# Kernel optimization log

Measured on AMD Instinct MI355X. Metric: run time of the kernel, lower is better.

Reference implementation:

```python
import jax, jax.numpy as jnp
import numpy as np

N = 65536        # total points across batch
NS = 16          # nsample (kNN neighbors)
D = 64           # d_model
FF = 64          # dim_feedforward width
CIN = 16         # input feature channels
EPS = 1e-5       # BatchNorm eps


def _bn_relu(x, g, b):
    # BatchNorm1d in training mode: per-channel stats over (N, L); x: (N, C, L)
    m = x.mean(axis=(0, 2), keepdims=True)
    v = x.var(axis=(0, 2), keepdims=True)
    return jax.nn.relu((x - m) * jax.lax.rsqrt(v + EPS) * g[None, :, None] + b[None, :, None])


def _dknn_layer(xyz, feats, knn_idx, knn_empty,
                wq, bq, wk, bk, w1, g1, b1, w2, g2, b2, wo, go, bo):
    # nhead = 1 -> single head uses the full d_model split
    Q = feats @ wq + bq                        # (N, D)
    K = feats @ wk + bk                        # (N, D)
    Kx = jnp.concatenate([K, xyz], axis=1)     # use_xyz=True -> (N, D+3)
    Qx = jnp.concatenate([Q, xyz], axis=1)     # (N, D+3)
    Kg = jnp.transpose(Kx[knn_idx], (0, 2, 1))  # irregular gather -> (N, D+3, NS)
    Qe = Qx[:, :, None]                        # (N, D+3, 1)
    x = jnp.concatenate([Kg - Qe, jnp.broadcast_to(Qe, Kg.shape)], axis=1)  # (N, 2*(D+3), NS)
    x = jnp.where(knn_empty[:, None, None], 0.0, x)   # empty-ball masking
    x = _bn_relu(jnp.einsum('ncs,cf->nfs', x, w1), g1, b1)  # Conv1d k=1 == channel matmul
    x = _bn_relu(jnp.einsum('ncs,cf->nfs', x, w2), g2, b2)
    x = jnp.max(x, axis=2, keepdims=True)      # max-pool over neighbors -> (N, FF, 1)
    x = _bn_relu(jnp.einsum('ncs,cf->nfs', x, wo), go, bo)  # out_conv
    return x[:, :, 0]                          # (N, D)


def setup_inputs() -> dict:
    key = jax.random.key(0)
    ks = jax.random.split(key, 16)
    inp = {
        'src_xyz': jax.random.normal(ks[0], (N, 3), jnp.float32) * 20.0,
        'src_feats': jax.random.normal(ks[1], (N, CIN), jnp.float32),
        'knn_idx': jax.random.randint(ks[2], (N, NS), 0, N, jnp.int32),
        'knn_empty': jax.random.randint(ks[3], (N,), 0, 20, jnp.int32) == 0,
    }
    k = 4
    cin = CIN
    for i in range(2):
        s = 1.0 / np.sqrt(cin)
        inp[f'l{i}_wq'] = jax.random.normal(ks[k], (cin, D), jnp.float32) * s; k += 1
        inp[f'l{i}_bq'] = jnp.zeros((D,), jnp.float32)
        inp[f'l{i}_wk'] = jax.random.normal(ks[k], (cin, D), jnp.float32) * s; k += 1
        inp[f'l{i}_bk'] = jnp.zeros((D,), jnp.float32)
        c = 2 * (D + 3)
        inp[f'l{i}_w1'] = jax.random.normal(ks[k], (c, FF), jnp.float32) * np.sqrt(2.0 / c); k += 1
        inp[f'l{i}_g1'] = jnp.ones((FF,), jnp.float32)
        inp[f'l{i}_b1'] = jnp.zeros((FF,), jnp.float32)
        inp[f'l{i}_w2'] = jax.random.normal(ks[k], (FF, FF), jnp.float32) * np.sqrt(2.0 / FF); k += 1
        inp[f'l{i}_g2'] = jnp.ones((FF,), jnp.float32)
        inp[f'l{i}_b2'] = jnp.zeros((FF,), jnp.float32)
        inp[f'l{i}_wo'] = jax.random.normal(ks[k], (FF, D), jnp.float32) * np.sqrt(2.0 / FF); k += 1
        inp[f'l{i}_go'] = jnp.ones((D,), jnp.float32)
        inp[f'l{i}_bo'] = jnp.zeros((D,), jnp.float32)
        cin = D
    return inp


def reference(src_xyz, src_feats, knn_idx, knn_empty,
              l0_wq, l0_bq, l0_wk, l0_bk, l0_w1, l0_g1, l0_b1, l0_w2, l0_g2, l0_b2, l0_wo, l0_go, l0_bo,
              l1_wq, l1_bq, l1_wk, l1_bk, l1_w1, l1_g1, l1_b1, l1_w2, l1_g2, l1_b2, l1_wo, l1_go, l1_bo):
    f = _dknn_layer(src_xyz, src_feats, knn_idx, knn_empty,
                    l0_wq, l0_bq, l0_wk, l0_bk, l0_w1, l0_g1, l0_b1, l0_w2, l0_g2, l0_b2, l0_wo, l0_go, l0_bo)
    f = _dknn_layer(src_xyz, f, knn_idx, knn_empty,
                    l1_wq, l1_bq, l1_wk, l1_bk, l1_w1, l1_g1, l1_b1, l1_w2, l1_g2, l1_b2, l1_wo, l1_go, l1_bo)
    return f
```

## Files before the change

kernel.cpp:

```cpp
#include <hip/hip_runtime.h>
#include <cstdint>

#define NPTS 65536
#define NS 16
#define EPSV 1e-5f

typedef __attribute__((ext_vector_type(8))) short bf16x8;
typedef __attribute__((ext_vector_type(4))) float f32x4;
typedef __attribute__((ext_vector_type(4))) unsigned int u32x4;
union FragU { u32x4 u; bf16x8 h; };

#define SUM1 0
#define SSQ1 64
#define SUM2 128
#define SSQ2 192
#define SUM3 256
#define SSQ3 320
#define WKAOF 0
#define WQBAOF 4096
#define BKAOF 8192
#define BQBAOF 8256
#define WFOLD_FLOATS 8320

__device__ __forceinline__ int permc(int c) {
    int t = c >> 5, g = (c >> 3) & 3, i = c & 7;
    return (t*2 + (i>>2))*16 + g*4 + (i&3);
}

__device__ __forceinline__ void split2(float e0, float e1, unsigned int& hi, unsigned int& lo) {
    unsigned int u0 = __float_as_uint(e0), u1 = __float_as_uint(e1);
    hi = __builtin_amdgcn_perm(u1, u0, 0x07060302u);
    float l0f = e0 - __uint_as_float(u0 & 0xFFFF0000u);
    float l1f = e1 - __uint_as_float(u1 & 0xFFFF0000u);
    lo = __builtin_amdgcn_perm(__float_as_uint(l1f), __float_as_uint(l0f), 0x07060302u);
}

__global__ void k_mask(const uint32_t* emp32, uint8_t* mask) {
    int bad = 0;
    for (int w = threadIdx.x; w < 1024; w += 256) bad |= (emp32[w] > 1u) ? 1 : 0;
    __shared__ int sbad[4];
    unsigned long long b = __ballot(bad != 0);
    if ((threadIdx.x & 63) == 0) sbad[threadIdx.x >> 6] = (b != 0ull) ? 1 : 0;
    __syncthreads();
    int flag = sbad[0] | sbad[1] | sbad[2] | sbad[3];
    int i = blockIdx.x * 256 + threadIdx.x;
    uint8_t mv;
    if (flag) mv = (((const uint8_t*)emp32)[i] != 0);
    else      mv = (emp32[i] != 0u);
    mask[i] = mv;
}

__global__ void k0(const float* wq, const float* bq, const float* wk, const float* bk,
                   const float* w1, float* wfold, int cin) {
    int f = threadIdx.x;
    int c = blockIdx.x;
    float a = 0.f, q = 0.f;
    for (int d = 0; d < 64; d++) {
        float A  = w1[d*64 + f];
        float Bm = w1[(67+d)*64 + f] - A;
        a = fmaf(wk[c*64 + d], A,  a);
        q = fmaf(wq[c*64 + d], Bm, q);
    }
    wfold[WKAOF  + c*64 + f] = a;
    wfold[WQBAOF + c*64 + f] = q;
    if (c == 0) {
        float ba = 0.f, bqv = 0.f;
        for (int d = 0; d < 64; d++) {
            float A  = w1[d*64 + f];
            float Bm = w1[(67+d)*64 + f] - A;
            ba  = fmaf(bk[d], A,  ba);
            bqv = fmaf(bq[d], Bm, bqv);
        }
        wfold[BKAOF  + f] = ba;
        wfold[BQBAOF + f] = bqv;
    }
}

template<int CIN, bool PREBN>
__global__ void __launch_bounds__(256) k1m(const float* __restrict__ feats, const float* __restrict__ xyz,
                    const float* __restrict__ w1, const float* __restrict__ wfold,
                    const float* __restrict__ statsPrev, const float* __restrict__ goP,
                    const float* __restrict__ boP,
                    float* __restrict__ KA, float* __restrict__ QBA) {
    const int l = threadIdx.x & 63;
    const int wv = threadIdx.x >> 6;
    const int sidx = l & 15;
    const int g = l >> 4;
    const int col = sidx;
    constexpr int NT = (CIN == 64) ? 2 : 1;

    unsigned int bh[NT][2][4], bl[NT][2][4];
    #pragma unroll
    for (int t = 0; t < NT; t++)
    #pragma unroll
    for (int fl = 0; fl < 2; fl++) {
        int f128 = (wv*2 + fl)*16 + col;
        const float* W = (f128 < 64) ? (wfold + WKAOF) : (wfold + WQBAOF);
        int f = (f128 < 64) ? f128 : f128 - 64;
        #pragma unroll
        for (int r = 0; r < 4; r++) {
            int c0 = t*32 + g*8 + 2*r;
            float e0 = 0.f, e1 = 0.f;
            if (CIN == 64 || g < 2) {
                e0 = W[c0*64 + f];
                e1 = W[(c0+1)*64 + f];
            }
            split2(e0, e1, bh[t][fl][r], bl[t][fl][r]);
        }
    }
    unsigned int xbh[2][4], xbl[2][4];
    float biasf[2];
    int posO[2];
    #pragma unroll
    for (int fl = 0; fl < 2; fl++) {
        int f128 = (wv*2 + fl)*16 + col;
        float A0, A1, A2;
        if (f128 < 64) {
            A0 = w1[64*64 + f128]; A1 = w1[65*64 + f128]; A2 = w1[66*64 + f128];
            biasf[fl] = wfold[BKAOF + f128];
            posO[fl] = permc(f128);
        } else {
            int f = f128 - 64;
            A0 = w1[131*64 + f] - w1[64*64 + f];
            A1 = w1[132*64 + f] - w1[65*64 + f];
            A2 = w1[133*64 + f] - w1[66*64 + f];
            biasf[fl] = wfold[BQBAOF + f];
            posO[fl] = permc(f);
        }
        split2(A0, A1, xbh[fl][0], xbl[fl][0]);
        split2(A2, 0.f, xbh[fl][1], xbl[fl][1]);
        xbh[fl][2] = 0; xbh[fl][3] = 0; xbl[fl][2] = 0; xbl[fl][3] = 0;
    }
    float scP[NT*8], shP[NT*8];
    if (PREBN) {
        const float invN = 1.0f / (float)NPTS;
        #pragma unroll
        for (int t = 0; t < NT; t++)
        #pragma unroll
        for (int i = 0; i < 8; i++) {
            int c = t*32 + g*8 + i;
            float m = statsPrev[SUM3 + c] * invN;
            float v = fmaxf(statsPrev[SSQ3 + c] * invN - m*m, 0.0f);
            float s = goP[c] * rsqrtf(v + EPSV);
            scP[t*8+i] = s;
            shP[t*8+i] = fmaf(-m, s, boP[c]);
        }
    }

    for (int tile = blockIdx.x; tile < NPTS/16; tile += gridDim.x) {
        int p = tile*16 + sidx;
        unsigned int ahu[NT][4], alu[NT][4];
        #pragma unroll
        for (int t = 0; t < NT; t++) {
            float xv[8];
            if (CIN == 64) {
                f32x4 a0 = *(const f32x4*)(feats + (size_t)p*64 + t*32 + g*8);
                f32x4 a1 = *(const f32x4*)(feats + (size_t)p*64 + t*32 + g*8 + 4);
                #pragma unroll
                for (int i = 0; i < 4; i++) { xv[i] = a0[i]; xv[4+i] = a1[i]; }
                if (PREBN) {
                    #pragma unroll
                    for (int i = 0; i < 8; i++)
                        xv[i] = fmaxf(fmaf(scP[t*8+i], xv[i], shP[t*8+i]), 0.0f);
                }
            } else {
                if (g < 2) {
                    f32x4 a0 = *(const f32x4*)(feats + (size_t)p*16 + g*8);
                    f32x4 a1 = *(const f32x4*)(feats + (size_t)p*16 + g*8 + 4);
                    #pragma unroll
                    for (int i = 0; i < 4; i++) { xv[i] = a0[i]; xv[4+i] = a1[i]; }
                } else {
                    #pragma unroll
                    for (int i = 0; i < 8; i++) xv[i] = 0.f;
                }
            }
            #pragma unroll
            for (int r = 0; r < 4; r++) split2(xv[2*r], xv[2*r+1], ahu[t][r], alu[t][r]);
        }
        unsigned int xah[4] = {0,0,0,0}, xal[4] = {0,0,0,0};
        if (g == 0) {
            float x0 = xyz[p*3], x1 = xyz[p*3+1], x2 = xyz[p*3+2];
            split2(x0, x1, xah[0], xal[0]);
            split2(x2, 0.f, xah[1], xal[1]);
        }
        f32x4 acc[2];
        #pragma unroll
        for (int fl = 0; fl < 2; fl++)
            acc[fl] = (f32x4){biasf[fl], biasf[fl], biasf[fl], biasf[fl]};
        #pragma unroll
        for (int t = 0; t < NT; t++) {
            FragU ah, al;
            ah.u = (u32x4){ahu[t][0], ahu[t][1], ahu[t][2], ahu[t][3]};
            al.u = (u32x4){alu[t][0], alu[t][1], alu[t][2], alu[t][3]};
            #pragma unroll
            for (int fl = 0; fl < 2; fl++) {
                FragU Bh, Bl;
                Bh.u = (u32x4){bh[t][fl][0], bh[t][fl][1], bh[t][fl][2], bh[t][fl][3]};
                Bl.u = (u32x4){bl[t][fl][0], bl[t][fl][1], bl[t][fl][2], bl[t][fl][3]};
                acc[fl] = __builtin_amdgcn_mfma_f32_16x16x32_bf16(ah.h, Bh.h, acc[fl], 0, 0, 0);
                acc[fl] = __builtin_amdgcn_mfma_f32_16x16x32_bf16(ah.h, Bl.h, acc[fl], 0, 0, 0);
                acc[fl] = __builtin_amdgcn_mfma_f32_16x16x32_bf16(al.h, Bh.h, acc[fl], 0, 0, 0);
            }
        }
        {
            FragU ah, al;
            ah.u = (u32x4){xah[0], xah[1], xah[2], xah[3]};
            al.u = (u32x4){xal[0], xal[1], xal[2], xal[3]};
            #pragma unroll
            for (int fl = 0; fl < 2; fl++) {
                FragU Bh, Bl;
                Bh.u = (u32x4){xbh[fl][0], xbh[fl][1], xbh[fl][2], xbh[fl][3]};
                Bl.u = (u32x4){xbl[fl][0], xbl[fl][1], xbl[fl][2], xbl[fl][3]};
                acc[fl] = __builtin_amdgcn_mfma_f32_16x16x32_bf16(ah.h, Bh.h, acc[fl], 0, 0, 0);
                acc[fl] = __builtin_amdgcn_mfma_f32_16x16x32_bf16(ah.h, Bl.h, acc[fl], 0, 0, 0);
                acc[fl] = __builtin_amdgcn_mfma_f32_16x16x32_bf16(al.h, Bh.h, acc[fl], 0, 0, 0);
            }
        }
        #pragma unroll
        for (int fl = 0; fl < 2; fl++) {
            int f128 = (wv*2 + fl)*16 + col;
            #pragma unroll
            for (int r = 0; r < 4; r++) {
                int po = tile*16 + g*4 + r;
                float v = acc[fl][r];
                if (f128 < 64) KA[(size_t)po*64 + posO[fl]] = v;
                else           QBA[(size_t)po*64 + posO[fl]] = v;
            }
        }
    }
}

__global__ void __launch_bounds__(256) k2(const float* __restrict__ KA, const float* __restrict__ QBA,
                   const int* __restrict__ knn, const uint8_t* __restrict__ mask, float* stats) {
    const int l = threadIdx.x & 63;
    const int wv = threadIdx.x >> 6;
    const int s = l & 15;
    const int g = l >> 4;
    float s0[16], s1[16];
    #pragma unroll
    for (int i = 0; i < 16; i++) { s0[i] = 0.f; s1[i] = 0.f; }

    const int STR = gridDim.x * 8;
    for (int n0 = blockIdx.x * 8 + wv*2; n0 < NPTS; n0 += STR) {
        bool msk[2];
        f32x4 ka[2][4];
        #pragma unroll
        for (int u = 0; u < 2; u++) {
            int n = n0 + u;
            msk[u] = (mask[n] != 0);
            if (!msk[u]) {
                int j = knn[n*16 + s];
                const float* kap = KA + (size_t)j*64 + g*4;
                #pragma unroll
                for (int q = 0; q < 4; q++) ka[u][q] = *(const f32x4*)(kap + q*16);
            }
        }
        #pragma unroll
        for (int u = 0; u < 2; u++) {
            if (msk[u]) continue;
            int n = n0 + u;
            const float* qbp = QBA + (size_t)n*64 + g*4;
            #pragma unroll
            for (int q = 0; q < 4; q++) {
                f32x4 qb = *(const f32x4*)(qbp + q*16);
                #pragma unroll
                for (int e = 0; e < 4; e++) {
                    float y = ka[u][q][e] + qb[e];
                    s0[q*4+e] += y;
                    s1[q*4+e] = fmaf(y, y, s1[q*4+e]);
                }
            }
        }
    }
    #pragma unroll
    for (int i = 0; i < 16; i++) {
        #pragma unroll
        for (int d = 1; d < 16; d <<= 1) {
            s0[i] += __shfl_xor(s0[i], d, 64);
            s1[i] += __shfl_xor(s1[i], d, 64);
        }
    }
    __shared__ float r0[4][64], r1[4][64];
    if (s == 0) {
        #pragma unroll
        for (int q = 0; q < 4; q++)
        #pragma unroll
        for (int e = 0; e < 4; e++) {
            int c = (q>>1)*32 + g*8 + (q&1)*4 + e;
            r0[wv][c] = s0[q*4+e];
            r1[wv][c] = s1[q*4+e];
        }
    }
    __syncthreads();
    int tid = threadIdx.x;
    if (tid < 64) {
        atomicAdd(&stats[SUM1 + tid], r0[0][tid]+r0[1][tid]+r0[2][tid]+r0[3][tid]);
        atomicAdd(&stats[SSQ1 + tid], r1[0][tid]+r1[1][tid]+r1[2][tid]+r1[3][tid]);
    }
}

__global__ void __launch_bounds__(256) k4(const float* __restrict__ KA, const float* __restrict__ QBA,
                   const int* __restrict__ knn, const uint8_t* __restrict__ mask,
                   const float* __restrict__ w2, const float* __restrict__ g1, const float* __restrict__ b1,
                   float* stats, float* __restrict__ y2max, float* __restrict__ y2min) {
    const int l    = threadIdx.x & 63;
    const int wv   = threadIdx.x >> 6;
    const int sidx = l & 15;
    const int g    = l >> 4;
    const int col  = sidx;

    float sc1v[16], sh1v[16];
    const float inv = 1.0f / ((float)NPTS * (float)NS);
    #pragma unroll
    for (int t = 0; t < 2; t++)
    #pragma unroll
    for (int i = 0; i < 8; i++) {
        int c = t*32 + g*8 + i;
        float m = stats[SUM1 + c] * inv;
        float v = fmaxf(stats[SSQ1 + c] * inv - m*m, 0.0f);
        float s = g1[c] * rsqrtf(v + EPSV);
        sc1v[t*8+i] = s;
        sh1v[t*8+i] = fmaf(-m, s, b1[c]);
    }

    unsigned int whu[2][4][4], wlu[2][4][4];
    #pragma unroll
    for (int t = 0; t < 2; t++)
    #pragma unroll
    for (int ft = 0; ft < 4; ft++)
    #pragma unroll
    for (int r = 0; r < 4; r++) {
        int k0i = t*32 + g*8 + 2*r;
        float e0 = w2[k0i*64 + ft*16 + col];
        float e1 = w2[(k0i+1)*64 + ft*16 + col];
        split2(e0, e1, whu[t][ft][r], wlu[t][ft][r]);
    }

    float s0t[4] = {0.f,0.f,0.f,0.f};
    float s1t[4] = {0.f,0.f,0.f,0.f};

    const int STR = gridDim.x * 8;
    for (int n0 = blockIdx.x * 8 + wv*2; n0 < NPTS; n0 += STR) {
        bool msk[2];
        f32x4 ka[2][4];
        #pragma unroll
        for (int u = 0; u < 2; u++) {
            int n = n0 + u;
            msk[u] = (mask[n] != 0);
            int j = knn[n*16 + sidx];
            const float* kap = KA + (size_t)j*64 + g*4;
            #pragma unroll
            for (int q = 0; q < 4; q++) ka[u][q] = *(const f32x4*)(kap + q*16);
        }
        #pragma unroll
        for (int u = 0; u < 2; u++) {
            int n = n0 + u;
            bool masked = msk[u];
            const float* qbp = QBA + (size_t)n*64 + g*4;
            f32x4 qq[4];
            #pragma unroll
            for (int q = 0; q < 4; q++) qq[q] = *(const f32x4*)(qbp + q*16);

            float x[16];
            #pragma unroll
            for (int t = 0; t < 2; t++)
            #pragma unroll
            for (int i = 0; i < 8; i++) {
                int q = t*2 + (i>>2), r = i&3;
                float y = masked ? 0.f : (ka[u][q][r] + qq[q][r]);
                x[t*8+i] = fmaxf(fmaf(sc1v[t*8+i], y, sh1v[t*8+i]), 0.0f);
            }

            unsigned int ahu[2][4], alu[2][4];
            #pragma unroll
            for (int t = 0; t < 2; t++)
            #pragma unroll
            for (int r = 0; r < 4; r++)
                split2(x[t*8 + 2*r], x[t*8 + 2*r + 1], ahu[t][r], alu[t][r]);

            f32x4 acc[4];
            #pragma unroll
            for (int ft = 0; ft < 4; ft++) acc[ft] = (f32x4){0.f,0.f,0.f,0.f};

            #pragma unroll
            for (int t = 0; t < 2; t++) {
                FragU ah, al;
                ah.u = (u32x4){ahu[t][0], ahu[t][1], ahu[t][2], ahu[t][3]};
                al.u = (u32x4){alu[t][0], alu[t][1], alu[t][2], alu[t][3]};
                #pragma unroll
                for (int ft = 0; ft < 4; ft++) {
                    FragU bhf, blf;
                    bhf.u = (u32x4){whu[t][ft][0], whu[t][ft][1], whu[t][ft][2], whu[t][ft][3]};
                    blf.u = (u32x4){wlu[t][ft][0], wlu[t][ft][1], wlu[t][ft][2], wlu[t][ft][3]};
                    acc[ft] = __builtin_amdgcn_mfma_f32_16x16x32_bf16(ah.h, bhf.h, acc[ft], 0, 0, 0);
                    acc[ft] = __builtin_amdgcn_mfma_f32_16x16x32_bf16(ah.h, blf.h, acc[ft], 0, 0, 0);
                    acc[ft] = __builtin_amdgcn_mfma_f32_16x16x32_bf16(al.h, bhf.h, acc[ft], 0, 0, 0);
                }
            }

            float tmax[4], tmin[4];
            #pragma unroll
            for (int ft = 0; ft < 4; ft++) {
                f32x4 d = acc[ft];
                float lmax = fmaxf(fmaxf(d[0], d[1]), fmaxf(d[2], d[3]));
                float lmin = fminf(fminf(d[0], d[1]), fminf(d[2], d[3]));
                s0t[ft] += (d[0] + d[1]) + (d[2] + d[3]);
                s1t[ft] += fmaf(d[0],d[0], fmaf(d[1],d[1], fmaf(d[2],d[2], d[3]*d[3])));
                lmax = fmaxf(lmax, __shfl_xor(lmax, 16, 64));
                lmax = fmaxf(lmax, __shfl_xor(lmax, 32, 64));
                lmin = fminf(lmin, __shfl_xor(lmin, 16, 64));
                lmin = fminf(lmin, __shfl_xor(lmin, 32, 64));
                tmax[ft] = lmax; tmin[ft] = lmin;
            }
            float mx = (g==0) ? tmax[0] : (g==1) ? tmax[1] : (g==2) ? tmax[2] : tmax[3];
            float mn = (g==0) ? tmin[0] : (g==1) ? tmin[1] : (g==2) ? tmin[2] : tmin[3];
            y2max[(size_t)n*64 + l] = mx;
            y2min[(size_t)n*64 + l] = mn;
        }
    }

    #pragma unroll
    for (int ft = 0; ft < 4; ft++) {
        s0t[ft] += __shfl_xor(s0t[ft], 16, 64);
        s0t[ft] += __shfl_xor(s0t[ft], 32, 64);
        s1t[ft] += __shfl_xor(s1t[ft], 16, 64);
        s1t[ft] += __shfl_xor(s1t[ft], 32, 64);
    }
    float myS0 = (g==0) ? s0t[0] : (g==1) ? s0t[1] : (g==2) ? s0t[2] : s0t[3];
    float myS1 = (g==0) ? s1t[0] : (g==1) ? s1t[1] : (g==2) ? s1t[2] : s1t[3];
    __shared__ float red[8][64];
    red[wv][l] = myS0;
    red[4+wv][l] = myS1;
    __syncthreads();
    if (wv == 0) {
        atomicAdd(&stats[SUM2 + l], red[0][l]+red[1][l]+red[2][l]+red[3][l]);
        atomicAdd(&stats[SSQ2 + l], red[4][l]+red[5][l]+red[6][l]+red[7][l]);
    }
}

__global__ void __launch_bounds__(256) k5m(const float* __restrict__ y2max, const float* __restrict__ y2min,
                    const float* __restrict__ wo, const float* __restrict__ g2, const float* __restrict__ b2,
                    float* stats, float* __restrict__ y3) {
    const int l = threadIdx.x & 63;
    const int wv = threadIdx.x >> 6;
    const int sidx = l & 15;
    const int g = l >> 4;
    const int ft = wv;

    unsigned int bh[2][4], bl[2][4];
    #pragma unroll
    for (int t = 0; t < 2; t++)
    #pragma unroll
    for (int r = 0; r < 4; r++) {
        int c0 = t*32 + g*8 + 2*r;
        split2(wo[c0*64 + ft*16 + sidx], wo[(c0+1)*64 + ft*16 + sidx], bh[t][r], bl[t][r]);
    }
    float sc2v[16], sh2v[16];
    const float inv = 1.0f / ((float)NPTS * (float)NS);
    #pragma unroll
    for (int t = 0; t < 2; t++)
    #pragma unroll
    for (int i = 0; i < 8; i++) {
        int c = t*32 + g*8 + i;
        float m = stats[SUM2 + c] * inv;
        float v = fmaxf(stats[SSQ2 + c] * inv - m*m, 0.0f);
        float s = g2[c] * rsqrtf(v + EPSV);
        sc2v[t*8+i] = s;
        sh2v[t*8+i] = fmaf(-m, s, b2[c]);
    }
    float s0a = 0.f, s1a = 0.f;
    for (int tile = blockIdx.x; tile < NPTS/16; tile += gridDim.x) {
        int p = tile*16 + sidx;
        unsigned int ahu[2][4], alu[2][4];
        #pragma unroll
        for (int t = 0; t < 2; t++) {
            f32x4 mx0 = *(const f32x4*)(y2max + (size_t)p*64 + t*32 + g*8);
            f32x4 mx1 = *(const f32x4*)(y2max + (size_t)p*64 + t*32 + g*8 + 4);
            f32x4 mn0 = *(const f32x4*)(y2min + (size_t)p*64 + t*32 + g*8);
            f32x4 mn1 = *(const f32x4*)(y2min + (size_t)p*64 + t*32 + g*8 + 4);
            float mval[8];
            #pragma unroll
            for (int i = 0; i < 4; i++) {
                float sc = sc2v[t*8+i];
                float pre = (sc >= 0.f) ? mx0[i] : mn0[i];
                mval[i] = fmaxf(fmaf(sc, pre, sh2v[t*8+i]), 0.0f);
                float sc2 = sc2v[t*8+4+i];
                float pre2 = (sc2 >= 0.f) ? mx1[i] : mn1[i];
                mval[4+i] = fmaxf(fmaf(sc2, pre2, sh2v[t*8+4+i]), 0.0f);
            }
            #pragma unroll
            for (int r = 0; r < 4; r++) split2(mval[2*r], mval[2*r+1], ahu[t][r], alu[t][r]);
        }
        f32x4 acc = (f32x4){0.f,0.f,0.f,0.f};
        #pragma unroll
        for (int t = 0; t < 2; t++) {
            FragU ah, al, Bh, Bl;
            ah.u = (u32x4){ahu[t][0], ahu[t][1], ahu[t][2], ahu[t][3]};
            al.u = (u32x4){alu[t][0], alu[t][1], alu[t][2], alu[t][3]};
            Bh.u = (u32x4){bh[t][0], bh[t][1], bh[t][2], bh[t][3]};
            Bl.u = (u32x4){bl[t][0], bl[t][1], bl[t][2], bl[t][3]};
            acc = __builtin_amdgcn_mfma_f32_16x16x32_bf16(ah.h, Bh.h, acc, 0, 0, 0);
            acc = __builtin_amdgcn_mfma_f32_16x16x32_bf16(ah.h, Bl.h, acc, 0, 0, 0);
            acc = __builtin_amdgcn_mfma_f32_16x16x32_bf16(al.h, Bh.h, acc, 0, 0, 0);
        }
        #pragma unroll
        for (int r = 0; r < 4; r++) {
            int po = tile*16 + g*4 + r;
            float v = acc[r];
            y3[(size_t)po*64 + ft*16 + sidx] = v;
            s0a += v;
            s1a = fmaf(v, v, s1a);
        }
    }
    s0a += __shfl_xor(s0a, 16, 64); s0a += __shfl_xor(s0a, 32, 64);
    s1a += __shfl_xor(s1a, 16, 64); s1a += __shfl_xor(s1a, 32, 64);
    __shared__ float r0[64], r1[64];
    if (l < 16) { r0[wv*16 + sidx] = s0a; r1[wv*16 + sidx] = s1a; }
    __syncthreads();
    int tid = threadIdx.x;
    if (tid < 64) {
        atomicAdd(&stats[SUM3 + tid], r0[tid]);
        atomicAdd(&stats[SSQ3 + tid], r1[tid]);
    }
}

__global__ void k6(float* y3, const float* stats, const float* go, const float* bo) {
    int i = blockIdx.x * 256 + threadIdx.x;
    int f = i & 63;
    const float inv = 1.0f / (float)NPTS;
    float m = stats[SUM3 + f] * inv;
    float v = fmaxf(stats[SSQ3 + f] * inv - m*m, 0.0f);
    float s = go[f] * rsqrtf(v + EPSV);
    float sh = fmaf(-m, s, bo[f]);
    y3[i] = fmaxf(fmaf(s, y3[i], sh), 0.0f);
}

extern "C" void kernel_launch(void* const* d_in, const int* in_sizes, int n_in,
                              void* d_out, int out_size, void* d_ws, size_t ws_size,
                              hipStream_t stream) {
    const float* xyz    = (const float*)d_in[0];
    const float* feats0 = (const float*)d_in[1];
    const int*   knn    = (const int*)d_in[2];
    const void*  empty  = d_in[3];
    float* ws = (float*)d_ws;
    const size_t N64 = (size_t)NPTS * 64;
    float* KA    = ws;
    float* QBA   = ws + N64;
    float* Y2MAX = ws + 2*N64;
    float* Y2MIN = ws + 3*N64;
    float* stats = ws + 4*N64;
    float* wfold = stats + 1024;
    uint8_t* mask = (uint8_t*)(wfold + WFOLD_FLOATS);
    float* out = (float*)d_out;

    hipMemsetAsync(stats, 0, 1024 * sizeof(float), stream);
    k_mask<<<NPTS/256, 256, 0, stream>>>((const uint32_t*)empty, mask);

    const float* const* p0 = (const float* const*)(d_in + 4);
    const float* const* p1 = (const float* const*)(d_in + 4 + 13);

    {
        const float* const* p = p0;
        float* sl = stats;
        k0<<<16, 64, 0, stream>>>(p[0], p[1], p[2], p[3], p[4], wfold, 16);
        k1m<16, false><<<1024, 256, 0, stream>>>(feats0, xyz, p[4], wfold,
                                                 sl, p[11], p[12], KA, QBA);
        k2<<<2048, 256, 0, stream>>>(KA, QBA, knn, mask, sl);
        k4<<<2048, 256, 0, stream>>>(KA, QBA, knn, mask, p[7], p[5], p[6], sl, Y2MAX, Y2MIN);
        k5m<<<2048, 256, 0, stream>>>(Y2MAX, Y2MIN, p[10], p[8], p[9], sl, out);
    }
    {
        const float* const* p = p1;
        float* sl = stats + 512;
        k0<<<64, 64, 0, stream>>>(p[0], p[1], p[2], p[3], p[4], wfold, 64);
        k1m<64, true><<<1024, 256, 0, stream>>>(out, xyz, p[4], wfold,
                                                stats, p0[11], p0[12], KA, QBA);
        k2<<<2048, 256, 0, stream>>>(KA, QBA, knn, mask, sl);
        k4<<<2048, 256, 0, stream>>>(KA, QBA, knn, mask, p[7], p[5], p[6], sl, Y2MAX, Y2MIN);
        k5m<<<2048, 256, 0, stream>>>(Y2MAX, Y2MIN, p[10], p[8], p[9], sl, out);
        k6<<<NPTS*64/256, 256, 0, stream>>>(out, sl, p[11], p[12]);
    }
}
```

Before: 608.7 us.

## Store gathered key projection KA in bf16 and drop the column permutation

The per-point key projection that is gathered irregularly through kNN indices is now written as bf16 instead of fp32, halving the bytes fetched per neighbour in the two gather-heavy kernels. The permuted column layout is replaced by natural order, and the loaders are rewritten to read 8 contiguous bf16 values per lane with matching QBA loads. The gather loops also process four points per wave iteration instead of two, so more loads are in flight. This loses precision in the BN statistics and the first-layer activations, since the key term is rounded to bf16 before the add.

New measurement: 581.9 us. 1.05x faster.

```diff
diff --git a/kernel.cpp b/kernel.cpp
--- a/kernel.cpp
+++ b/kernel.cpp
@@ -6,6 +6,7 @@
 #define EPSV 1e-5f
 
 typedef __attribute__((ext_vector_type(8))) short bf16x8;
+typedef __attribute__((ext_vector_type(8))) unsigned short u16x8;
 typedef __attribute__((ext_vector_type(4))) float f32x4;
 typedef __attribute__((ext_vector_type(4))) unsigned int u32x4;
 union FragU { u32x4 u; bf16x8 h; };
@@ -22,17 +23,21 @@
 #define BQBAOF 8256
 #define WFOLD_FLOATS 8320
 
-__device__ __forceinline__ int permc(int c) {
-    int t = c >> 5, g = (c >> 3) & 3, i = c & 7;
-    return (t*2 + (i>>2))*16 + g*4 + (i&3);
-}
-
 __device__ __forceinline__ void split2(float e0, float e1, unsigned int& hi, unsigned int& lo) {
     unsigned int u0 = __float_as_uint(e0), u1 = __float_as_uint(e1);
     hi = __builtin_amdgcn_perm(u1, u0, 0x07060302u);
     float l0f = e0 - __uint_as_float(u0 & 0xFFFF0000u);
     float l1f = e1 - __uint_as_float(u1 & 0xFFFF0000u);
     lo = __builtin_amdgcn_perm(__float_as_uint(l1f), __float_as_uint(l0f), 0x07060302u);
+}
+
+__device__ __forceinline__ unsigned short f2bf(float x) {
+    unsigned int u = __float_as_uint(x);
+    u += 0x7FFFu + ((u >> 16) & 1u);
+    return (unsigned short)(u >> 16);
+}
+__device__ __forceinline__ float bf2f(unsigned short h) {
+    return __uint_as_float(((unsigned int)h) << 16);
 }
 
 __global__ void k_mask(const uint32_t* emp32, uint8_t* mask) {
@@ -81,7 +86,7 @@
                     const float* __restrict__ w1, const float* __restrict__ wfold,
                     const float* __restrict__ statsPrev, const float* __restrict__ goP,
                     const float* __restrict__ boP,
-                    float* __restrict__ KA, float* __restrict__ QBA) {
+                    unsigned short* __restrict__ KAb, float* __restrict__ QBA) {
     const int l = threadIdx.x & 63;
     const int wv = threadIdx.x >> 6;
     const int sidx = l & 15;
@@ -110,7 +115,6 @@
     }
     unsigned int xbh[2][4], xbl[2][4];
     float biasf[2];
-    int posO[2];
     #pragma unroll
     for (int fl = 0; fl < 2; fl++) {
         int f128 = (wv*2 + fl)*16 + col;
@@ -118,14 +122,12 @@
         if (f128 < 64) {
             A0 = w1[64*64 + f128]; A1 = w1[65*64 + f128]; A2 = w1[66*64 + f128];
             biasf[fl] = wfold[BKAOF + f128];
-            posO[fl] = permc(f128);
         } else {
             int f = f128 - 64;
             A0 = w1[131*64 + f] - w1[64*64 + f];
             A1 = w1[132*64 + f] - w1[65*64 + f];
             A2 = w1[133*64 + f] - w1[66*64 + f];
             biasf[fl] = wfold[BQBAOF + f];
-            posO[fl] = permc(f);
         }
         split2(A0, A1, xbh[fl][0], xbl[fl][0]);
         split2(A2, 0.f, xbh[fl][1], xbl[fl][1]);
@@ -223,14 +225,14 @@
             for (int r = 0; r < 4; r++) {
                 int po = tile*16 + g*4 + r;
                 float v = acc[fl][r];
-                if (f128 < 64) KA[(size_t)po*64 + posO[fl]] = v;
-                else           QBA[(size_t)po*64 + posO[fl]] = v;
-            }
-        }
-    }
-}
-
-__global__ void __launch_bounds__(256) k2(const float* __restrict__ KA, const float* __restrict__ QBA,
+                if (f128 < 64) KAb[(size_t)po*64 + f128] = f2bf(v);
+                else           QBA[(size_t)po*64 + (f128-64)] = v;
+            }
+        }
+    }
+}
+
+__global__ void __launch_bounds__(256) k2(const unsigned short* __restrict__ KAb, const float* __restrict__ QBA,
                    const int* __restrict__ knn, const uint8_t* __restrict__ mask, float* stats) {
     const int l = threadIdx.x & 63;
     const int wv = threadIdx.x >> 6;
@@ -240,35 +242,40 @@
     #pragma unroll
     for (int i = 0; i < 16; i++) { s0[i] = 0.f; s1[i] = 0.f; }
 
-    const int STR = gridDim.x * 8;
-    for (int n0 = blockIdx.x * 8 + wv*2; n0 < NPTS; n0 += STR) {
-        bool msk[2];
-        f32x4 ka[2][4];
-        #pragma unroll
-        for (int u = 0; u < 2; u++) {
+    const int STR = gridDim.x * 16;
+    for (int n0 = blockIdx.x * 16 + wv*4; n0 < NPTS; n0 += STR) {
+        bool msk[4];
+        u16x8 ka[4][2];
+        #pragma unroll
+        for (int u = 0; u < 4; u++) {
             int n = n0 + u;
             msk[u] = (mask[n] != 0);
             if (!msk[u]) {
                 int j = knn[n*16 + s];
-                const float* kap = KA + (size_t)j*64 + g*4;
-                #pragma unroll
-                for (int q = 0; q < 4; q++) ka[u][q] = *(const f32x4*)(kap + q*16);
-            }
-        }
-        #pragma unroll
-        for (int u = 0; u < 2; u++) {
+                const unsigned short* kp = KAb + (size_t)j*64;
+                ka[u][0] = *(const u16x8*)(kp + g*8);
+                ka[u][1] = *(const u16x8*)(kp + 32 + g*8);
+            }
+        }
+        #pragma unroll
+        for (int u = 0; u < 4; u++) {
             if (msk[u]) continue;
             int n = n0 + u;
-            const float* qbp = QBA + (size_t)n*64 + g*4;
-            #pragma unroll
-            for (int q = 0; q < 4; q++) {
-                f32x4 qb = *(const f32x4*)(qbp + q*16);
-                #pragma unroll
-                for (int e = 0; e < 4; e++) {
-                    float y = ka[u][q][e] + qb[e];
-                    s0[q*4+e] += y;
-                    s1[q*4+e] = fmaf(y, y, s1[q*4+e]);
-                }
+            const float* qp = QBA + (size_t)n*64;
+            f32x4 q0 = *(const f32x4*)(qp + g*8);
+            f32x4 q1 = *(const f32x4*)(qp + g*8 + 4);
+            f32x4 q2 = *(const f32x4*)(qp + 32 + g*8);
+            f32x4 q3 = *(const f32x4*)(qp + 32 + g*8 + 4);
+            #pragma unroll
+            for (int t = 0; t < 2; t++)
+            #pragma unroll
+            for (int i = 0; i < 8; i++) {
+                float kf = bf2f(ka[u][t][i]);
+                float qv = t ? ((i < 4) ? q2[i] : q3[i-4])
+                             : ((i < 4) ? q0[i] : q1[i-4]);
+                float y = kf + qv;
+                s0[t*8+i] += y;
+                s1[t*8+i] = fmaf(y, y, s1[t*8+i]);
             }
         }
     }
@@ -283,12 +290,12 @@
     __shared__ float r0[4][64], r1[4][64];
     if (s == 0) {
         #pragma unroll
-        for (int q = 0; q < 4; q++)
-        #pragma unroll
-        for (int e = 0; e < 4; e++) {
-            int c = (q>>1)*32 + g*8 + (q&1)*4 + e;
-            r0[wv][c] = s0[q*4+e];
-            r1[wv][c] = s1[q*4+e];
+        for (int t = 0; t < 2; t++)
+        #pragma unroll
+        for (int i = 0; i < 8; i++) {
+            int c = t*32 + g*8 + i;
+            r0[wv][c] = s0[t*8+i];
+            r1[wv][c] = s1[t*8+i];
         }
     }
     __syncthreads();
@@ -299,7 +306,7 @@
     }
 }
 
-__global__ void __launch_bounds__(256) k4(const float* __restrict__ KA, const float* __restrict__ QBA,
+__global__ void __launch_bounds__(256) k4(const unsigned short* __restrict__ KAb, const float* __restrict__ QBA,
                    const int* __restrict__ knn, const uint8_t* __restrict__ mask,
                    const float* __restrict__ w2, const float* __restrict__ g1, const float* __restrict__ b1,
                    float* stats, float* __restrict__ y2max, float* __restrict__ y2min) {
@@ -339,35 +346,38 @@
     float s0t[4] = {0.f,0.f,0.f,0.f};
     float s1t[4] = {0.f,0.f,0.f,0.f};
 
-    const int STR = gridDim.x * 8;
-    for (int n0 = blockIdx.x * 8 + wv*2; n0 < NPTS; n0 += STR) {
-        bool msk[2];
-        f32x4 ka[2][4];
-        #pragma unroll
-        for (int u = 0; u < 2; u++) {
+    const int STR = gridDim.x * 16;
+    for (int n0 = blockIdx.x * 16 + wv*4; n0 < NPTS; n0 += STR) {
+        bool msk[4];
+        u16x8 ka[4][2];
+        #pragma unroll
+        for (int u = 0; u < 4; u++) {
             int n = n0 + u;
             msk[u] = (mask[n] != 0);
             int j = knn[n*16 + sidx];
-            const float* kap = KA + (size_t)j*64 + g*4;
-            #pragma unroll
-            for (int q = 0; q < 4; q++) ka[u][q] = *(const f32x4*)(kap + q*16);
-        }
-        #pragma unroll
-        for (int u = 0; u < 2; u++) {
+            const unsigned short* kp = KAb + (size_t)j*64;
+            ka[u][0] = *(const u16x8*)(kp + g*8);
+            ka[u][1] = *(const u16x8*)(kp + 32 + g*8);
+        }
+        #pragma unroll
+        for (int u = 0; u < 4; u++) {
             int n = n0 + u;
             bool masked = msk[u];
-            const float* qbp = QBA + (size_t)n*64 + g*4;
-            f32x4 qq[4];
-            #pragma unroll
-            for (int q = 0; q < 4; q++) qq[q] = *(const f32x4*)(qbp + q*16);
+            const float* qp = QBA + (size_t)n*64;
+            f32x4 q0 = *(const f32x4*)(qp + g*8);
+            f32x4 q1 = *(const f32x4*)(qp + g*8 + 4);
+            f32x4 q2 = *(const f32x4*)(qp + 32 + g*8);
+            f32x4 q3 = *(const f32x4*)(qp + 32 + g*8 + 4);
 
             float x[16];
             #pragma unroll
             for (int t = 0; t < 2; t++)
             #pragma unroll
             for (int i = 0; i < 8; i++) {
-                int q = t*2 + (i>>2), r = i&3;
-                float y = masked ? 0.f : (ka[u][q][r] + qq[q][r]);
+                float kf = bf2f(ka[u][t][i]);
+                float qv = t ? ((i < 4) ? q2[i] : q3[i-4])
+                             : ((i < 4) ? q0[i] : q1[i-4]);
+                float y = masked ? 0.f : (kf + qv);
                 x[t*8+i] = fmaxf(fmaf(sc1v[t*8+i], y, sh1v[t*8+i]), 0.0f);
             }
 
@@ -544,7 +554,7 @@
     const void*  empty  = d_in[3];
     float* ws = (float*)d_ws;
     const size_t N64 = (size_t)NPTS * 64;
-    float* KA    = ws;
+    unsigned short* KAb = (unsigned short*)ws;
     float* QBA   = ws + N64;
     float* Y2MAX = ws + 2*N64;
     float* Y2MIN = ws + 3*N64;
@@ -564,9 +574,9 @@
         float* sl = stats;
         k0<<<16, 64, 0, stream>>>(p[0], p[1], p[2], p[3], p[4], wfold, 16);
         k1m<16, false><<<1024, 256, 0, stream>>>(feats0, xyz, p[4], wfold,
-                                                 sl, p[11], p[12], KA, QBA);
-        k2<<<2048, 256, 0, stream>>>(KA, QBA, knn, mask, sl);
-        k4<<<2048, 256, 0, stream>>>(KA, QBA, knn, mask, p[7], p[5], p[6], sl, Y2MAX, Y2MIN);
+                                                 sl, p[11], p[12], KAb, QBA);
+        k2<<<2048, 256, 0, stream>>>(KAb, QBA, knn, mask, sl);
+        k4<<<2048, 256, 0, stream>>>(KAb, QBA, knn, mask, p[7], p[5], p[6], sl, Y2MAX, Y2MIN);
         k5m<<<2048, 256, 0, stream>>>(Y2MAX, Y2MIN, p[10], p[8], p[9], sl, out);
     }
     {
@@ -574,9 +584,9 @@
         float* sl = stats + 512;
         k0<<<64, 64, 0, stream>>>(p[0], p[1], p[2], p[3], p[4], wfold, 64);
         k1m<64, true><<<1024, 256, 0, stream>>>(out, xyz, p[4], wfold,
-                                                stats, p0[11], p0[12], KA, QBA);
-        k2<<<2048, 256, 0, stream>>>(KA, QBA, knn, mask, sl);
-        k4<<<2048, 256, 0, stream>>>(KA, QBA, knn, mask, p[7], p[5], p[6], sl, Y2MAX, Y2MIN);
+                                                stats, p0[11], p0[12], KAb, QBA);
+        k2<<<2048, 256, 0, stream>>>(KAb, QBA, knn, mask, sl);
+        k4<<<2048, 256, 0, stream>>>(KAb, QBA, knn, mask, p[7], p[5], p[6], sl, Y2MAX, Y2MIN);
         k5m<<<2048, 256, 0, stream>>>(Y2MAX, Y2MIN, p[10], p[8], p[9], sl, out);
         k6<<<NPTS*64/256, 256, 0, stream>>>(out, sl, p[11], p[12]);
     }
```
